# Performance work log

Measured on AMD Instinct MI355X. Metric: run time of the kernel, lower is better.

## Reference

```python
import jax, jax.numpy as jnp
import numpy as np

NUM_NODES = 50000
NUM_EDGES = 800000
DIM = 64
NUM_REL2 = 400
NUM_LAYERS = 3
NUM_TAILS = 512


def setup_inputs() -> dict:
    key = jax.random.key(0)
    ks = jax.random.split(key, 16)
    s = lambda shape, k, scale: jax.random.normal(k, shape, jnp.float32) * scale
    return {
        'head_embeds': s((DIM,), ks[0], 1.0),
        'rel_table': s((NUM_REL2, DIM), ks[1], 0.1),
        'rel_W': s((NUM_LAYERS, NUM_REL2, DIM), ks[2], 0.1),
        'agg_W': s((NUM_LAYERS, 8 * DIM, DIM), ks[3], (8 * DIM) ** -0.5),
        'agg_b': jnp.zeros((NUM_LAYERS, DIM), jnp.float32),
        'lin_W': s((2 * DIM, DIM), ks[4], (2 * DIM) ** -0.5),
        'lin_b': jnp.zeros((DIM,), jnp.float32),
        'mlp_W1': s((DIM, 2 * DIM), ks[5], DIM ** -0.5),
        'mlp_b1': jnp.zeros((2 * DIM,), jnp.float32),
        'mlp_W2': s((2 * DIM, 1), ks[6], (2 * DIM) ** -0.5),
        'mlp_b2': jnp.zeros((1,), jnp.float32),
        'edge_src': jax.random.randint(ks[7], (NUM_EDGES,), 0, NUM_NODES, jnp.int32),
        'edge_dst': jax.random.randint(ks[8], (NUM_EDGES,), 0, NUM_NODES, jnp.int32),
        'edge_type': jax.random.randint(ks[9], (NUM_EDGES,), 0, NUM_REL2, jnp.int32),
        'head_index': 0,
        'r_index': 7,
        't_index': jax.random.randint(ks[10], (NUM_TAILS,), 0, NUM_NODES, jnp.int32),
    }


def _score_fn(hidden, query, lin_W, lin_b, mlp_W1, mlp_b1, mlp_W2, mlp_b2):
    # hidden: [N, d], query: [d]
    q = jnp.broadcast_to(query, hidden.shape)
    heuristic = jnp.concatenate([hidden, q], axis=-1) @ lin_W + lin_b  # [N, d]
    x = hidden * heuristic
    h1 = jax.nn.relu(x @ mlp_W1 + mlp_b1)
    return (h1 @ mlp_W2 + mlp_b2)[..., 0]  # [N]


def reference(head_embeds, rel_table, rel_W, agg_W, agg_b, lin_W, lin_b,
              mlp_W1, mlp_b1, mlp_W2, mlp_b2,
              edge_src, edge_dst, edge_type, head_index, r_index, t_index):
    N, d = NUM_NODES, DIM
    score_fn = lambda h, q: _score_fn(h, q, lin_W, lin_b, mlp_W1, mlp_b1, mlp_W2, mlp_b2)

    query = rel_table[r_index]  # [d]

    # init_input_embeds: boundary zeros except head node; init score
    hidden = jnp.zeros((N, d), jnp.float32).at[head_index].set(head_embeds)
    zero_s = score_fn(jnp.zeros((1, d), jnp.float32), query)[0]
    score = jnp.full((N,), zero_s, jnp.float32)
    score = score.at[head_index].set(score_fn(head_embeds[None, :], query)[0])
    score = jnp.clip(score, -15.0, 15.0)

    deg = jax.ops.segment_sum(jnp.ones_like(edge_dst, jnp.float32), edge_dst, N)  # [N]
    deg_safe = jnp.maximum(deg, 1.0)
    has_in = deg > 0
    pna_degree_mean = jnp.log(deg + 1.0).mean()
    scale = (jnp.log(deg + 1.0) / pna_degree_mean)[:, None]  # [N,1]

    for l in range(NUM_LAYERS):
        gate = jax.nn.sigmoid(score)[:, None]  # [N,1]
        layer_input = gate * hidden  # [N,d]
        # relational messages: gather + per-relation transform
        msg = layer_input[edge_src] * rel_W[l][edge_type]  # [E,d]
        # PNA aggregators per destination node
        ssum = jax.ops.segment_sum(msg, edge_dst, N)
        mean = ssum / deg_safe[:, None]
        sq = jax.ops.segment_sum(msg * msg, edge_dst, N) / deg_safe[:, None]
        std = jnp.sqrt(jnp.maximum(sq - mean * mean, 0.0) + 1e-6)
        mx = jax.ops.segment_max(msg, edge_dst, N)
        mn = jax.ops.segment_min(msg, edge_dst, N)
        mx = jnp.where(has_in[:, None], mx, 0.0)
        mn = jnp.where(has_in[:, None], mn, 0.0)
        feat = jnp.concatenate([mean, mx, mn, std], axis=-1)  # [N,4d]
        feat = jnp.concatenate([feat, feat * scale], axis=-1)  # [N,8d]
        update = feat @ agg_W[l] + agg_b[l]  # [N,d]
        # residual update only for nodes with incoming edges
        hidden = hidden + jnp.where(has_in[:, None], update, 0.0)
        new_score = score_fn(hidden, query)
        score = jnp.where(has_in, new_score, score)

    return score[t_index]  # [NUM_TAILS]
```

## Files before the change

kernel.cpp:

```cpp
#include <hip/hip_runtime.h>
#include <math.h>

#define NN 50000
#define NREL 400
#define NLAYERS 3

static __device__ __forceinline__ float clip15(float x) { return fminf(fmaxf(x, -15.f), 15.f); }

static __device__ __forceinline__ unsigned short f2bf(float f) {
  unsigned u = __float_as_uint(f);
  unsigned r = (u + 0x7FFFu + ((u >> 16) & 1u)) >> 16;
  return (unsigned short)r;
}
static __device__ __forceinline__ float bf2f(unsigned short s) {
  return __uint_as_float(((unsigned)s) << 16);
}

typedef __attribute__((ext_vector_type(8))) short bf16x8;
typedef __attribute__((ext_vector_type(4))) float f32x4;

__global__ void count_k(const int* __restrict__ dst, int* __restrict__ deg, int E) {
  int e = blockIdx.x * blockDim.x + threadIdx.x;
  if (e < E) atomicAdd(&deg[dst[e]], 1);
}

__global__ void scan_k(const int* __restrict__ deg, int* __restrict__ start, int* __restrict__ cursor,
                       int* __restrict__ counter, float* __restrict__ logsum, int N) {
  int n = blockIdx.x * blockDim.x + threadIdx.x;
  int lane = threadIdx.x & 63;
  int d = (n < N) ? deg[n] : 0;
  int pre = d;
  #pragma unroll
  for (int off = 1; off < 64; off <<= 1) { int t = __shfl_up(pre, off); if (lane >= off) pre += t; }
  int base = 0;
  if (lane == 63) base = atomicAdd(counter, pre);
  base = __shfl(base, 63);
  if (n < N) { int pos = base + pre - d; start[n] = pos; cursor[n] = pos; }
  float v = (n < N) ? logf((float)d + 1.0f) : 0.f;
  #pragma unroll
  for (int off = 32; off; off >>= 1) v += __shfl_xor(v, off);
  if (lane == 0) atomicAdd(logsum, v);
}

__global__ void scale_k(const int* __restrict__ deg, const float* __restrict__ logsum,
                        float* __restrict__ scale, int N) {
  int n = blockIdx.x * blockDim.x + threadIdx.x;
  if (n < N) scale[n] = logf((float)deg[n] + 1.0f) * (float)N / logsum[0];
}

__global__ void scatter_k(const int* __restrict__ src, const int* __restrict__ dst,
                          const int* __restrict__ typ, int* __restrict__ cursor,
                          int2* __restrict__ csr, int E) {
  int e = blockIdx.x * blockDim.x + threadIdx.x;
  if (e < E) {
    int dd = dst[e];
    int pos = atomicAdd(&cursor[dd], 1);
    csr[pos] = make_int2(src[e], typ[e]);
  }
}

__global__ void wconv_k(const float* __restrict__ aggW, unsigned short* __restrict__ WT) {
  int idx = blockIdx.x * blockDim.x + threadIdx.x;
  if (idx >= 3 * 64 * 256) return;
  int k = idx & 255;
  int out = (idx >> 8) & 63;
  int l = idx >> 14;
  const float* Wl = aggW + (size_t)l * 512 * 64;
  float wa = Wl[(size_t)k * 64 + out];
  float wb = Wl[(size_t)(256 + k) * 64 + out];
  unsigned short wah = f2bf(wa);
  unsigned short wal = f2bf(wa - bf2f(wah));
  unsigned short wbh = f2bf(wb);
  unsigned short wbl = f2bf(wb - bf2f(wbh));
  unsigned short* WTl = WT + (size_t)l * 4 * 64 * 256;
  WTl[((size_t)0 * 64 + out) * 256 + k] = wah;
  WTl[((size_t)1 * 64 + out) * 256 + k] = wal;
  WTl[((size_t)2 * 64 + out) * 256 + k] = wbh;
  WTl[((size_t)3 * 64 + out) * 256 + k] = wbl;
}

__global__ void prep_k(const float* __restrict__ head_embeds, const float* __restrict__ rel_table,
                       const float* __restrict__ lin_W, const float* __restrict__ lin_b,
                       const float* __restrict__ mlp_W1, const float* __restrict__ mlp_b1,
                       const float* __restrict__ mlp_W2, const float* __restrict__ mlp_b2,
                       const int* __restrict__ head_index, const int* __restrict__ r_index,
                       float* __restrict__ hidden, float* __restrict__ scalars) {
  int j = threadIdx.x;
  int r = r_index[0], hd = head_index[0];
  float qj = rel_table[r * 64 + j];
  float cq = lin_b[j];
  for (int k = 0; k < 64; ++k) cq += __shfl(qj, k) * lin_W[(64 + k) * 64 + j];
  scalars[j] = cq;
  float t = fmaxf(mlp_b1[j], 0.f) * mlp_W2[j] + fmaxf(mlp_b1[64 + j], 0.f) * mlp_W2[64 + j];
  #pragma unroll
  for (int off = 32; off; off >>= 1) t += __shfl_xor(t, off);
  float zs = clip15(t + mlp_b2[0]);
  float hj = head_embeds[j];
  hidden[(size_t)hd * 64 + j] = hj;
  float heur = cq;
  for (int k = 0; k < 64; ++k) heur += __shfl(hj, k) * lin_W[k * 64 + j];
  float xj = hj * heur;
  float h1a = mlp_b1[j], h1b = mlp_b1[64 + j];
  for (int k = 0; k < 64; ++k) {
    float xk = __shfl(xj, k);
    h1a += xk * mlp_W1[k * 128 + j];
    h1b += xk * mlp_W1[k * 128 + 64 + j];
  }
  h1a = fmaxf(h1a, 0.f); h1b = fmaxf(h1b, 0.f);
  float p = h1a * mlp_W2[j] + h1b * mlp_W2[64 + j];
  #pragma unroll
  for (int off = 32; off; off >>= 1) p += __shfl_xor(p, off);
  float hs = clip15(p + mlp_b2[0]);
  if (j == 0) { scalars[64] = zs; scalars[65] = hs; }
}

__global__ void fill_k(float* __restrict__ score, const float* __restrict__ scalars,
                       const int* __restrict__ head_index, int N) {
  int n = blockIdx.x * blockDim.x + threadIdx.x;
  if (n < N) score[n] = (n == head_index[0]) ? scalars[65] : scalars[64];
}

__global__ void gate_k(const float* __restrict__ hidden, const float* __restrict__ score,
                       float* __restrict__ LI, int N) {
  int i = blockIdx.x * blockDim.x + threadIdx.x;
  if (i < N * 16) {
    int node = i >> 4;
    float s = score[node];
    float g = 1.f / (1.f + expf(-s));
    float4 h = ((const float4*)hidden)[i];
    float4 r = make_float4(h.x * g, h.y * g, h.z * g, h.w * g);
    ((float4*)LI)[i] = r;
  }
}

__global__ __launch_bounds__(256) void agg_k(const float* __restrict__ LI, const int2* __restrict__ csr,
                                             const int* __restrict__ start, const int* __restrict__ deg,
                                             const float* __restrict__ relW, float* __restrict__ f1, int N) {
  int wid = threadIdx.x >> 6;
  int lane = threadIdx.x & 63;
  int node = blockIdx.x * 4 + wid;
  if (node >= N) return;
  int base = start[node], d = deg[node];
  float sum = 0.f, sq = 0.f, mx = -3.402823e38f, mn = 3.402823e38f;
  int e = 0;
  for (; e + 8 <= d; e += 8) {
    int2 p[8];
    #pragma unroll
    for (int i = 0; i < 8; ++i) p[i] = csr[base + e + i];
    float m[8];
    #pragma unroll
    for (int i = 0; i < 8; ++i) {
      float a = LI[p[i].x * 64 + lane];
      float w = relW[p[i].y * 64 + lane];
      m[i] = a * w;
    }
    #pragma unroll
    for (int i = 0; i < 8; ++i) {
      sum += m[i]; sq += m[i] * m[i];
      mx = fmaxf(mx, m[i]); mn = fminf(mn, m[i]);
    }
  }
  for (; e + 4 <= d; e += 4) {
    int2 p0 = csr[base + e], p1 = csr[base + e + 1];
    int2 p2 = csr[base + e + 2], p3 = csr[base + e + 3];
    float a0 = LI[p0.x * 64 + lane], w0 = relW[p0.y * 64 + lane];
    float a1 = LI[p1.x * 64 + lane], w1 = relW[p1.y * 64 + lane];
    float a2 = LI[p2.x * 64 + lane], w2 = relW[p2.y * 64 + lane];
    float a3 = LI[p3.x * 64 + lane], w3 = relW[p3.y * 64 + lane];
    float m0 = a0 * w0, m1 = a1 * w1, m2 = a2 * w2, m3 = a3 * w3;
    sum += (m0 + m1) + (m2 + m3);
    sq += (m0 * m0 + m1 * m1) + (m2 * m2 + m3 * m3);
    mx = fmaxf(fmaxf(mx, fmaxf(m0, m1)), fmaxf(m2, m3));
    mn = fminf(fminf(mn, fminf(m0, m1)), fminf(m2, m3));
  }
  for (; e < d; ++e) {
    int2 p = csr[base + e];
    float m = LI[p.x * 64 + lane] * relW[p.y * 64 + lane];
    sum += m; sq += m * m; mx = fmaxf(mx, m); mn = fminf(mn, m);
  }
  float* out = f1 + (size_t)node * 256;
  if (d > 0) {
    float inv = 1.0f / (float)d;
    float mean = sum * inv, sqm = sq * inv;
    float sd = sqrtf(fmaxf(sqm - mean * mean, 0.f) + 1e-6f);
    out[lane] = mean; out[64 + lane] = mx; out[128 + lane] = mn; out[192 + lane] = sd;
  } else {
    out[lane] = 0.f; out[64 + lane] = 0.f; out[128 + lane] = 0.f; out[192 + lane] = 0.f;
  }
}

#define KP 40
__global__ __launch_bounds__(256) void gemm_k(const float* __restrict__ f1,
                                              const unsigned short* __restrict__ WT,
                                              const float* __restrict__ aggb, const float* __restrict__ scale,
                                              const int* __restrict__ deg, float* __restrict__ hidden, int N) {
  __shared__ __align__(16) unsigned short sA[2][64 * KP];
  __shared__ __align__(16) unsigned short sW[4][64 * KP];
  int tid = threadIdx.x;
  int wv = tid >> 6;
  int l = tid & 63;
  int lrow = l & 15;
  int lhi = l >> 4;
  int n0 = blockIdx.x * 64;

  f32x4 acc[8];
  #pragma unroll
  for (int i = 0; i < 8; ++i) acc[i] = (f32x4){0.f, 0.f, 0.f, 0.f};

  int anode = tid >> 2;
  int akq = (tid & 3) * 8;
  bool avalid = (n0 + anode) < N;
  const float* Arow = f1 + (size_t)(n0 + anode) * 256 + akq;

  for (int kc = 0; kc < 8; ++kc) {
    float fv[8];
    if (avalid) {
      float4 v0 = *(const float4*)(Arow + kc * 32);
      float4 v1 = *(const float4*)(Arow + kc * 32 + 4);
      fv[0] = v0.x; fv[1] = v0.y; fv[2] = v0.z; fv[3] = v0.w;
      fv[4] = v1.x; fv[5] = v1.y; fv[6] = v1.z; fv[7] = v1.w;
    } else {
      #pragma unroll
      for (int j = 0; j < 8; ++j) fv[j] = 0.f;
    }
    unsigned int ph[4], pl[4];
    #pragma unroll
    for (int j = 0; j < 4; ++j) {
      unsigned short h0 = f2bf(fv[2 * j]),     l0 = f2bf(fv[2 * j] - bf2f(h0));
      unsigned short h1 = f2bf(fv[2 * j + 1]), l1 = f2bf(fv[2 * j + 1] - bf2f(h1));
      ph[j] = (unsigned)h0 | ((unsigned)h1 << 16);
      pl[j] = (unsigned)l0 | ((unsigned)l1 << 16);
    }
    *(uint4*)&sA[0][anode * KP + akq] = make_uint4(ph[0], ph[1], ph[2], ph[3]);
    *(uint4*)&sA[1][anode * KP + akq] = make_uint4(pl[0], pl[1], pl[2], pl[3]);
    {
      int wrow = tid >> 2;
      int wkq = (tid & 3) * 8;
      #pragma unroll
      for (int p = 0; p < 4; ++p) {
        const unsigned short* src = WT + ((size_t)p * 64 + wrow) * 256 + kc * 32 + wkq;
        *(uint4*)&sW[p][wrow * KP + wkq] = *(const uint4*)src;
      }
    }
    __syncthreads();
    {
      int arow = (wv * 16 + lrow) * KP + lhi * 8;
      bf16x8 ah = *(const bf16x8*)&sA[0][arow];
      bf16x8 al = *(const bf16x8*)&sA[1][arow];
      #pragma unroll
      for (int t = 0; t < 4; ++t) {
        int wr = (t * 16 + lrow) * KP + lhi * 8;
        bf16x8 wah = *(const bf16x8*)&sW[0][wr];
        bf16x8 wal = *(const bf16x8*)&sW[1][wr];
        acc[t] = __builtin_amdgcn_mfma_f32_16x16x32_bf16(ah, wah, acc[t], 0, 0, 0);
        acc[t] = __builtin_amdgcn_mfma_f32_16x16x32_bf16(ah, wal, acc[t], 0, 0, 0);
        acc[t] = __builtin_amdgcn_mfma_f32_16x16x32_bf16(al, wah, acc[t], 0, 0, 0);
        bf16x8 wbh = *(const bf16x8*)&sW[2][wr];
        bf16x8 wbl = *(const bf16x8*)&sW[3][wr];
        acc[4 + t] = __builtin_amdgcn_mfma_f32_16x16x32_bf16(ah, wbh, acc[4 + t], 0, 0, 0);
        acc[4 + t] = __builtin_amdgcn_mfma_f32_16x16x32_bf16(ah, wbl, acc[4 + t], 0, 0, 0);
        acc[4 + t] = __builtin_amdgcn_mfma_f32_16x16x32_bf16(al, wbh, acc[4 + t], 0, 0, 0);
      }
    }
    __syncthreads();
  }

  #pragma unroll
  for (int r = 0; r < 4; ++r) {
    int node = n0 + wv * 16 + lhi * 4 + r;
    if (node < N && deg[node] > 0) {
      float sc = scale[node];
      #pragma unroll
      for (int t = 0; t < 4; ++t) {
        int out = t * 16 + lrow;
        float* hp = &hidden[(size_t)node * 64 + out];
        *hp += acc[t][r] + sc * acc[4 + t][r] + aggb[out];
      }
    }
  }
}

#define SC_LDS 12992
__global__ __launch_bounds__(256) void score2_k(const float* __restrict__ hidden, float* __restrict__ score,
                                                const int* __restrict__ deg, const float* __restrict__ lin_W,
                                                const float* __restrict__ mlp_W1, const float* __restrict__ mlp_b1,
                                                const float* __restrict__ mlp_W2, const float* __restrict__ mlp_b2,
                                                const float* __restrict__ scalars, int N) {
  __shared__ float smem[SC_LDS];
  float* X   = smem;
  float* H   = smem + 4160;
  float* WA  = smem + 8320;
  float* W1s = smem + 4160;
  float* sW2 = smem + 12416;
  float* sb1 = smem + 12544;
  float* scq = smem + 12672;
  float* pred= smem + 12736;

  int t = threadIdx.x;
  int lane = t & 63;
  int g = t >> 6;
  int n0 = blockIdx.x * 64;

  for (int i = t; i < 1024; i += 256) ((float4*)WA)[i] = ((const float4*)lin_W)[i];
  if (t < 128) { sW2[t] = mlp_W2[t]; sb1[t] = mlp_b1[t]; }
  if (t < 64) scq[t] = scalars[t];
  for (int i = t; i < 1024; i += 256) {
    int node = i >> 4;
    int k4 = (i & 15) << 2;
    float4 v = make_float4(0.f, 0.f, 0.f, 0.f);
    if (n0 + node < N) v = ((const float4*)(hidden + (size_t)(n0 + node) * 64))[i & 15];
    float* hp = &H[node * 65 + k4];
    hp[0] = v.x; hp[1] = v.y; hp[2] = v.z; hp[3] = v.w;
  }
  __syncthreads();

  float acc[16];
  #pragma unroll
  for (int i = 0; i < 16; ++i) acc[i] = scq[g * 16 + i];
  #pragma unroll 8
  for (int kk = 0; kk < 64; ++kk) {
    float h = H[lane * 65 + kk];
    const float4* wr = (const float4*)&WA[kk * 64 + g * 16];
    float4 w0 = wr[0], w1 = wr[1], w2 = wr[2], w3 = wr[3];
    acc[0]  += h * w0.x; acc[1]  += h * w0.y; acc[2]  += h * w0.z; acc[3]  += h * w0.w;
    acc[4]  += h * w1.x; acc[5]  += h * w1.y; acc[6]  += h * w1.z; acc[7]  += h * w1.w;
    acc[8]  += h * w2.x; acc[9]  += h * w2.y; acc[10] += h * w2.z; acc[11] += h * w2.w;
    acc[12] += h * w3.x; acc[13] += h * w3.y; acc[14] += h * w3.z; acc[15] += h * w3.w;
  }
  #pragma unroll
  for (int i = 0; i < 16; ++i) {
    int j = g * 16 + i;
    X[lane * 65 + j] = H[lane * 65 + j] * acc[i];
  }
  __syncthreads();

  for (int i = t; i < 2048; i += 256) ((float4*)W1s)[i] = ((const float4*)mlp_W1)[i];
  __syncthreads();

  float acc2[32];
  #pragma unroll
  for (int i = 0; i < 32; ++i) acc2[i] = sb1[g * 32 + i];
  #pragma unroll 4
  for (int kk = 0; kk < 64; ++kk) {
    float xv = X[lane * 65 + kk];
    const float4* wr = (const float4*)&W1s[kk * 128 + g * 32];
    #pragma unroll
    for (int s = 0; s < 8; ++s) {
      float4 w = wr[s];
      acc2[s * 4 + 0] += xv * w.x; acc2[s * 4 + 1] += xv * w.y;
      acc2[s * 4 + 2] += xv * w.z; acc2[s * 4 + 3] += xv * w.w;
    }
  }
  float p = 0.f;
  #pragma unroll
  for (int i = 0; i < 32; ++i) p += fmaxf(acc2[i], 0.f) * sW2[g * 32 + i];
  pred[g * 64 + lane] = p;
  __syncthreads();
  if (t < 64) {
    int node = n0 + t;
    if (node < N && deg[node] > 0)
      score[node] = pred[t] + pred[64 + t] + pred[128 + t] + pred[192 + t] + mlp_b2[0];
  }
}

__global__ void out_k(const float* __restrict__ score, const int* __restrict__ t_index,
                      float* __restrict__ out, int T) {
  int i = blockIdx.x * blockDim.x + threadIdx.x;
  if (i < T) out[i] = score[t_index[i]];
}

extern "C" void kernel_launch(void* const* d_in, const int* in_sizes, int n_in,
                              void* d_out, int out_size, void* d_ws, size_t ws_size,
                              hipStream_t stream) {
  const float* head_embeds = (const float*)d_in[0];
  const float* rel_table   = (const float*)d_in[1];
  const float* rel_W       = (const float*)d_in[2];
  const float* agg_W       = (const float*)d_in[3];
  const float* agg_b       = (const float*)d_in[4];
  const float* lin_W       = (const float*)d_in[5];
  const float* lin_b       = (const float*)d_in[6];
  const float* mlp_W1      = (const float*)d_in[7];
  const float* mlp_b1      = (const float*)d_in[8];
  const float* mlp_W2      = (const float*)d_in[9];
  const float* mlp_b2      = (const float*)d_in[10];
  const int* edge_src      = (const int*)d_in[11];
  const int* edge_dst      = (const int*)d_in[12];
  const int* edge_type     = (const int*)d_in[13];
  const int* head_index    = (const int*)d_in[14];
  const int* r_index       = (const int*)d_in[15];
  const int* t_index       = (const int*)d_in[16];
  int E = in_sizes[11];
  int T = in_sizes[16];
  int N = NN;

  char* w = (char*)d_ws;
  size_t off = 0;
  auto alloc = [&](size_t bytes) {
    void* p = w + off;
    off = (off + bytes + 255) & ~(size_t)255;
    return p;
  };
  int* deg      = (int*)alloc((size_t)N * 4);
  int* start    = (int*)alloc((size_t)N * 4);
  int* cursor   = (int*)alloc((size_t)N * 4);
  float* scale  = (float*)alloc((size_t)N * 4);
  int* counter  = (int*)alloc(4);
  float* logsum = (float*)alloc(4);
  float* scalars= (float*)alloc(66 * 4);
  int2* csr     = (int2*)alloc((size_t)E * 8);
  float* hidden = (float*)alloc((size_t)N * 64 * 4);
  float* score  = (float*)alloc((size_t)N * 4);
  float* LI     = (float*)alloc((size_t)N * 64 * 4);
  float* f1     = (float*)alloc((size_t)N * 256 * 4);
  unsigned short* WT = (unsigned short*)alloc((size_t)3 * 4 * 64 * 256 * 2);
  if (off > ws_size) return;

  hipMemsetAsync(deg, 0, (size_t)N * 4, stream);
  hipMemsetAsync(counter, 0, 4, stream);
  hipMemsetAsync(logsum, 0, 4, stream);
  hipMemsetAsync(hidden, 0, (size_t)N * 64 * 4, stream);

  count_k<<<(E + 255) / 256, 256, 0, stream>>>(edge_dst, deg, E);
  scan_k<<<(N + 255) / 256, 256, 0, stream>>>(deg, start, cursor, counter, logsum, N);
  scale_k<<<(N + 255) / 256, 256, 0, stream>>>(deg, logsum, scale, N);
  scatter_k<<<(E + 255) / 256, 256, 0, stream>>>(edge_src, edge_dst, edge_type, cursor, csr, E);
  wconv_k<<<(3 * 64 * 256 + 255) / 256, 256, 0, stream>>>(agg_W, WT);
  prep_k<<<1, 64, 0, stream>>>(head_embeds, rel_table, lin_W, lin_b, mlp_W1, mlp_b1, mlp_W2, mlp_b2,
                               head_index, r_index, hidden, scalars);
  fill_k<<<(N + 255) / 256, 256, 0, stream>>>(score, scalars, head_index, N);

  for (int l = 0; l < NLAYERS; ++l) {
    gate_k<<<(N * 16 + 255) / 256, 256, 0, stream>>>(hidden, score, LI, N);
    agg_k<<<(N + 3) / 4, 256, 0, stream>>>(LI, csr, start, deg, rel_W + (size_t)l * NREL * 64, f1, N);
    gemm_k<<<(N + 63) / 64, 256, 0, stream>>>(f1, WT + (size_t)l * 4 * 64 * 256,
                                              agg_b + (size_t)l * 64, scale, deg, hidden, N);
    score2_k<<<(N + 63) / 64, 256, 0, stream>>>(hidden, score, deg, lin_W, mlp_W1, mlp_b1, mlp_W2, mlp_b2,
                                                scalars, N);
  }
  out_k<<<(T + 255) / 256, 256, 0, stream>>>(score, t_index, (float*)d_out, T);
}
```

Before: 504.2 us.

## Fuse sigmoid gating into aggregation and emit split-bf16 features from agg

Replaces the per-element gate kernel with a per-node sigmoid kernel and applies the gate inside the edge-gather loop, so the gated copy of hidden (LI) is never written or re-read. The aggregation kernel now writes its features directly as hi/lo bf16 pairs, and the GEMM loads them without converting. Byte traffic for the feature buffer stays the same, but conversion work moves out of the GEMM. The cost is an extra scalar gate load per edge in the gather loop, and the hi/lo conversion is now done in agg_k with 2-byte scattered stores.

```diff
diff --git a/kernel.cpp b/kernel.cpp
--- a/kernel.cpp
+++ b/kernel.cpp
@@ -120,22 +120,17 @@
   if (n < N) score[n] = (n == head_index[0]) ? scalars[65] : scalars[64];
 }
 
-__global__ void gate_k(const float* __restrict__ hidden, const float* __restrict__ score,
-                       float* __restrict__ LI, int N) {
-  int i = blockIdx.x * blockDim.x + threadIdx.x;
-  if (i < N * 16) {
-    int node = i >> 4;
-    float s = score[node];
-    float g = 1.f / (1.f + expf(-s));
-    float4 h = ((const float4*)hidden)[i];
-    float4 r = make_float4(h.x * g, h.y * g, h.z * g, h.w * g);
-    ((float4*)LI)[i] = r;
-  }
-}
-
-__global__ __launch_bounds__(256) void agg_k(const float* __restrict__ LI, const int2* __restrict__ csr,
+__global__ void gsig_k(const float* __restrict__ score, float* __restrict__ gate, int N) {
+  int n = blockIdx.x * blockDim.x + threadIdx.x;
+  if (n < N) gate[n] = 1.f / (1.f + expf(-score[n]));
+}
+
+__global__ __launch_bounds__(256) void agg_k(const float* __restrict__ hidden, const float* __restrict__ gate,
+                                             const int2* __restrict__ csr,
                                              const int* __restrict__ start, const int* __restrict__ deg,
-                                             const float* __restrict__ relW, float* __restrict__ f1, int N) {
+                                             const float* __restrict__ relW,
+                                             unsigned short* __restrict__ f1h, unsigned short* __restrict__ f1l,
+                                             int N) {
   int wid = threadIdx.x >> 6;
   int lane = threadIdx.x & 63;
   int node = blockIdx.x * 4 + wid;
@@ -150,9 +145,9 @@
     float m[8];
     #pragma unroll
     for (int i = 0; i < 8; ++i) {
-      float a = LI[p[i].x * 64 + lane];
+      float li = gate[p[i].x] * hidden[p[i].x * 64 + lane];
       float w = relW[p[i].y * 64 + lane];
-      m[i] = a * w;
+      m[i] = li * w;
     }
     #pragma unroll
     for (int i = 0; i < 8; ++i) {
@@ -163,10 +158,10 @@
   for (; e + 4 <= d; e += 4) {
     int2 p0 = csr[base + e], p1 = csr[base + e + 1];
     int2 p2 = csr[base + e + 2], p3 = csr[base + e + 3];
-    float a0 = LI[p0.x * 64 + lane], w0 = relW[p0.y * 64 + lane];
-    float a1 = LI[p1.x * 64 + lane], w1 = relW[p1.y * 64 + lane];
-    float a2 = LI[p2.x * 64 + lane], w2 = relW[p2.y * 64 + lane];
-    float a3 = LI[p3.x * 64 + lane], w3 = relW[p3.y * 64 + lane];
+    float a0 = gate[p0.x] * hidden[p0.x * 64 + lane], w0 = relW[p0.y * 64 + lane];
+    float a1 = gate[p1.x] * hidden[p1.x * 64 + lane], w1 = relW[p1.y * 64 + lane];
+    float a2 = gate[p2.x] * hidden[p2.x * 64 + lane], w2 = relW[p2.y * 64 + lane];
+    float a3 = gate[p3.x] * hidden[p3.x * 64 + lane], w3 = relW[p3.y * 64 + lane];
     float m0 = a0 * w0, m1 = a1 * w1, m2 = a2 * w2, m3 = a3 * w3;
     sum += (m0 + m1) + (m2 + m3);
     sq += (m0 * m0 + m1 * m1) + (m2 * m2 + m3 * m3);
@@ -175,22 +170,31 @@
   }
   for (; e < d; ++e) {
     int2 p = csr[base + e];
-    float m = LI[p.x * 64 + lane] * relW[p.y * 64 + lane];
+    float li = gate[p.x] * hidden[p.x * 64 + lane];
+    float m = li * relW[p.y * 64 + lane];
     sum += m; sq += m * m; mx = fmaxf(mx, m); mn = fminf(mn, m);
   }
-  float* out = f1 + (size_t)node * 256;
+  unsigned short* oh = f1h + (size_t)node * 256;
+  unsigned short* ol = f1l + (size_t)node * 256;
+  float v0, v1, v2, v3;
   if (d > 0) {
     float inv = 1.0f / (float)d;
     float mean = sum * inv, sqm = sq * inv;
     float sd = sqrtf(fmaxf(sqm - mean * mean, 0.f) + 1e-6f);
-    out[lane] = mean; out[64 + lane] = mx; out[128 + lane] = mn; out[192 + lane] = sd;
+    v0 = mean; v1 = mx; v2 = mn; v3 = sd;
   } else {
-    out[lane] = 0.f; out[64 + lane] = 0.f; out[128 + lane] = 0.f; out[192 + lane] = 0.f;
-  }
+    v0 = 0.f; v1 = 0.f; v2 = 0.f; v3 = 0.f;
+  }
+  unsigned short h0 = f2bf(v0), h1 = f2bf(v1), h2 = f2bf(v2), h3 = f2bf(v3);
+  oh[lane] = h0;        ol[lane] = f2bf(v0 - bf2f(h0));
+  oh[64 + lane] = h1;   ol[64 + lane] = f2bf(v1 - bf2f(h1));
+  oh[128 + lane] = h2;  ol[128 + lane] = f2bf(v2 - bf2f(h2));
+  oh[192 + lane] = h3;  ol[192 + lane] = f2bf(v3 - bf2f(h3));
 }
 
 #define KP 40
-__global__ __launch_bounds__(256) void gemm_k(const float* __restrict__ f1,
+__global__ __launch_bounds__(256) void gemm_k(const unsigned short* __restrict__ f1h,
+                                              const unsigned short* __restrict__ f1l,
                                               const unsigned short* __restrict__ WT,
                                               const float* __restrict__ aggb, const float* __restrict__ scale,
                                               const int* __restrict__ deg, float* __restrict__ hidden, int N) {
@@ -210,29 +214,17 @@
   int anode = tid >> 2;
   int akq = (tid & 3) * 8;
   bool avalid = (n0 + anode) < N;
-  const float* Arow = f1 + (size_t)(n0 + anode) * 256 + akq;
+  const unsigned short* Ah = f1h + (size_t)(n0 + anode) * 256 + akq;
+  const unsigned short* Al = f1l + (size_t)(n0 + anode) * 256 + akq;
 
   for (int kc = 0; kc < 8; ++kc) {
-    float fv[8];
+    uint4 vh = make_uint4(0, 0, 0, 0), vl = vh;
     if (avalid) {
-      float4 v0 = *(const float4*)(Arow + kc * 32);
-      float4 v1 = *(const float4*)(Arow + kc * 32 + 4);
-      fv[0] = v0.x; fv[1] = v0.y; fv[2] = v0.z; fv[3] = v0.w;
-      fv[4] = v1.x; fv[5] = v1.y; fv[6] = v1.z; fv[7] = v1.w;
-    } else {
-      #pragma unroll
-      for (int j = 0; j < 8; ++j) fv[j] = 0.f;
-    }
-    unsigned int ph[4], pl[4];
-    #pragma unroll
-    for (int j = 0; j < 4; ++j) {
-      unsigned short h0 = f2bf(fv[2 * j]),     l0 = f2bf(fv[2 * j] - bf2f(h0));
-      unsigned short h1 = f2bf(fv[2 * j + 1]), l1 = f2bf(fv[2 * j + 1] - bf2f(h1));
-      ph[j] = (unsigned)h0 | ((unsigned)h1 << 16);
-      pl[j] = (unsigned)l0 | ((unsigned)l1 << 16);
-    }
-    *(uint4*)&sA[0][anode * KP + akq] = make_uint4(ph[0], ph[1], ph[2], ph[3]);
-    *(uint4*)&sA[1][anode * KP + akq] = make_uint4(pl[0], pl[1], pl[2], pl[3]);
+      vh = *(const uint4*)(Ah + kc * 32);
+      vl = *(const uint4*)(Al + kc * 32);
+    }
+    *(uint4*)&sA[0][anode * KP + akq] = vh;
+    *(uint4*)&sA[1][anode * KP + akq] = vl;
     {
       int wrow = tid >> 2;
       int wkq = (tid & 3) * 8;
@@ -410,8 +402,9 @@
   int2* csr     = (int2*)alloc((size_t)E * 8);
   float* hidden = (float*)alloc((size_t)N * 64 * 4);
   float* score  = (float*)alloc((size_t)N * 4);
-  float* LI     = (float*)alloc((size_t)N * 64 * 4);
-  float* f1     = (float*)alloc((size_t)N * 256 * 4);
+  float* gate   = (float*)alloc((size_t)N * 4);
+  unsigned short* f1h = (unsigned short*)alloc((size_t)N * 256 * 2);
+  unsigned short* f1l = (unsigned short*)alloc((size_t)N * 256 * 2);
   unsigned short* WT = (unsigned short*)alloc((size_t)3 * 4 * 64 * 256 * 2);
   if (off > ws_size) return;
 
@@ -430,9 +423,10 @@
   fill_k<<<(N + 255) / 256, 256, 0, stream>>>(score, scalars, head_index, N);
 
   for (int l = 0; l < NLAYERS; ++l) {
-    gate_k<<<(N * 16 + 255) / 256, 256, 0, stream>>>(hidden, score, LI, N);
-    agg_k<<<(N + 3) / 4, 256, 0, stream>>>(LI, csr, start, deg, rel_W + (size_t)l * NREL * 64, f1, N);
-    gemm_k<<<(N + 63) / 64, 256, 0, stream>>>(f1, WT + (size_t)l * 4 * 64 * 256,
+    gsig_k<<<(N + 255) / 256, 256, 0, stream>>>(score, gate, N);
+    agg_k<<<(N + 3) / 4, 256, 0, stream>>>(hidden, gate, csr, start, deg,
+                                           rel_W + (size_t)l * NREL * 64, f1h, f1l, N);
+    gemm_k<<<(N + 63) / 64, 256, 0, stream>>>(f1h, f1l, WT + (size_t)l * 4 * 64 * 256,
                                               agg_b + (size_t)l * 64, scale, deg, hidden, N);
     score2_k<<<(N + 63) / 64, 256, 0, stream>>>(hidden, score, deg, lin_W, mlp_W1, mlp_b1, mlp_W2, mlp_b2,
                                                 scalars, N);
```

Measured after the change: 524.1 us. 3.9% more time.
